# Kernel optimization log

Hardware: AMD Instinct MI355X
Metric: run time of the kernel (lower is better)

## Reference

```python
import jax, jax.numpy as jnp
import numpy as np

N_NODES = 100000
N_EDGES = 1600000
D = 128


def setup_inputs() -> dict:
    key = jax.random.key(0)
    ks = jax.random.split(key, 6)
    x = jax.random.normal(ks[0], (N_NODES, D), dtype=jnp.float32)
    edge_index = jax.random.randint(ks[1], (2, N_EDGES), 0, N_NODES, dtype=jnp.int32)
    # nn.Linear weights: [out, in], bias [out]
    W1 = jax.random.normal(ks[2], (D, D), dtype=jnp.float32) * (1.0 / np.sqrt(D))
    b1 = jax.random.normal(ks[3], (D,), dtype=jnp.float32) * 0.01
    W2 = jax.random.normal(ks[4], (D, D), dtype=jnp.float32) * (1.0 / np.sqrt(D))
    b2 = jax.random.normal(ks[5], (D,), dtype=jnp.float32) * 0.01
    return {"x": x, "edge_index": edge_index, "W1": W1, "b1": b1, "W2": W2, "b2": b2}


def _gin_conv(x, src, dst, W, b, num_nodes):
    # sum aggregation of source features into destination nodes
    agg = jax.ops.segment_sum(x[src], dst, num_segments=num_nodes)  # [N, d]
    # eps = 0 (PyG GINConv default): (1+eps)*x_i + sum_j x_j, then Linear
    return (x + agg) @ W.T + b


def reference(x, edge_index, W1, b1, W2, b2):
    src, dst = edge_index[0], edge_index[1]
    n = x.shape[0]
    hid = _gin_conv(x, src, dst, W1, b1, n)
    out = _gin_conv(hid, src, dst, W2, b2, n)
    return (out, hid)
```

## Files before the change

### kernel.cpp

```cpp
#include <hip/hip_runtime.h>


#define DFEAT 128
#define BSHIFT 8
#define NB_MAX 512
#define CAP 8192
#define LROWS 136

typedef __attribute__((ext_vector_type(8))) short short8;
typedef __attribute__((ext_vector_type(4))) float f32x4;

__device__ __forceinline__ float bf2f(unsigned short u) {
    union { unsigned int i; float f; } c;
    c.i = ((unsigned int)u) << 16;
    return c.f;
}
__device__ __forceinline__ unsigned short f2b(float f) {
    union { float f; unsigned int i; } c;
    c.f = f;
    unsigned int u = c.i;
    u = (u + 0x7FFFu + ((u >> 16) & 1u)) >> 16;
    return (unsigned short)u;
}


__global__ __launch_bounds__(256) void scatter_cast(const int* __restrict__ src,
                                                    const int* __restrict__ dst,
                                                    int* __restrict__ bcur,
                                                    int* __restrict__ ebuf, int E,
                                                    int nscat,
                                                    const float* __restrict__ x,
                                                    unsigned short* __restrict__ xb,
                                                    int total4, int nzero) {
    int tid = threadIdx.x;
    if (blockIdx.x >= nscat) {
        int i = (blockIdx.x - nscat) * 256 + tid;
        if (i < total4) {
            float4 v = ((const float4*)x)[i];
            ushort4 o;
            o.x = f2b(v.x); o.y = f2b(v.y); o.z = f2b(v.z); o.w = f2b(v.w);
            ((ushort4*)xb)[i] = o;
        }
        if (blockIdx.x == nscat && tid < 32)
            ((ushort4*)xb)[(size_t)nzero * 32 + tid] = make_ushort4(0, 0, 0, 0);
        return;
    }
    __shared__ int lh[NB_MAX];
    for (int i = tid; i < NB_MAX; i += 256) lh[i] = 0;
    __syncthreads();
    int e0 = blockIdx.x * 4096;
    int e1 = min(e0 + 4096, E);
    int s[16], d[16];
    #pragma unroll
    for (int j = 0; j < 16; j++) {
        int e = e0 + tid + 256 * j;
        if (e < e1) { s[j] = src[e]; d[j] = dst[e]; atomicAdd(&lh[d[j] >> BSHIFT], 1); }
    }
    __syncthreads();
    for (int i = tid; i < NB_MAX; i += 256) {
        int c = lh[i];
        lh[i] = c ? (i * CAP + atomicAdd(&bcur[i], c)) : 0;
    }
    __syncthreads();
    #pragma unroll
    for (int j = 0; j < 16; j++) {
        int e = e0 + tid + 256 * j;
        if (e < e1) {
            int b = d[j] >> BSHIFT;
            int p = atomicAdd(&lh[b], 1);
            if (p < (b + 1) * CAP) ebuf[p] = (s[j] << 8) | (d[j] & 255);
        }
    }
}


__global__ __launch_bounds__(256) void csr_prep(const int* __restrict__ ebuf,
                                                const int* __restrict__ bcur,
                                                int2* __restrict__ rpse,
                                                int* __restrict__ esrc, int n, int nbk,
                                                const float* __restrict__ W1,
                                                const float* __restrict__ W2,
                                                const float* __restrict__ b1,
                                                unsigned short* __restrict__ Wb1,
                                                unsigned short* __restrict__ Wcb,
                                                float* __restrict__ w2b1) {
    int tid = threadIdx.x;
    if (blockIdx.x >= nbk) {
        __shared__ float red[256];
        int bb = blockIdx.x - nbk;
        int i = bb * 2 + (tid >> 7);
        int j = tid & 127;
        float s = 0.f;
        #pragma unroll 4
        for (int k = 0; k < 128; k++) s += W2[i * 128 + k] * W1[k * 128 + j];
        Wcb[i * 128 + j] = f2b(s);
        Wb1[i * 128 + j] = f2b(W1[i * 128 + j]);
        red[tid] = W2[i * 128 + j] * b1[j];
        __syncthreads();
        if (j == 0) {
            float t = 0.f;
            for (int k = 0; k < 128; k++) t += red[tid + k];
            w2b1[i] = t;
        }
        return;
    }
    __shared__ int hist[256];
    __shared__ int wsum[4];
    __shared__ int woff2[4];
    int b = blockIdx.x;
    int nbase = b << BSHIFT;
    int e0 = b * CAP;
    int e1 = e0 + min(bcur[b], CAP);
    hist[tid] = 0;
    __syncthreads();
    for (int e = e0 + tid; e < e1; e += 256)
        atomicAdd(&hist[ebuf[e] & 255], 1);
    __syncthreads();
    int v = hist[tid];
    int lane = tid & 63, wid = tid >> 6;
    int inc = v;
    #pragma unroll
    for (int off = 1; off < 64; off <<= 1) {
        int u = __shfl_up(inc, off, 64);
        if (lane >= off) inc += u;
    }
    if (lane == 63) wsum[wid] = inc;
    __syncthreads();
    if (tid == 0) {
        int run = 0;
        #pragma unroll
        for (int w = 0; w < 4; w++) { woff2[w] = run; run += wsum[w]; }
    }
    __syncthreads();
    int excl = woff2[wid] + inc - v;
    int node = nbase + tid;
    if (node < n) rpse[node] = make_int2(e0 + excl, e0 + excl + v);
    __syncthreads();
    hist[tid] = excl;
    __syncthreads();
    for (int e = e0 + tid; e < e1; e += 256) {
        int le = ebuf[e];
        int p = atomicAdd(&hist[le & 255], 1);
        esrc[e0 + p] = ((unsigned int)le) >> 8;
    }
}


__device__ __forceinline__ void agg_node16(const char* __restrict__ zb,
                                           const int2* __restrict__ rpse,
                                           const int* __restrict__ esrc,
                                           int node, int nzero, int gl, int gbase,
                                           unsigned lb, float a[8]) {
    int2 se = rpse[node];
    int e0 = se.x, deg = se.y - se.x;
    short8 sv = *(const short8*)(zb + (unsigned)node * 256u + lb);
    #pragma unroll
    for (int t = 0; t < 8; t++) a[t] = bf2f((unsigned short)sv[t]);

    int ei0 = (gl < deg) ? esrc[e0 + gl] : nzero;
    int ei1 = (gl + 16 < deg) ? esrc[e0 + gl + 16] : nzero;

    {
        unsigned off[16];
        short8 vv[16];
        #pragma unroll
        for (int k = 0; k < 16; k++)
            off[k] = (unsigned)__shfl(ei0, gbase + k) * 256u + lb;
        #pragma unroll
        for (int k = 0; k < 16; k++) vv[k] = *(const short8*)(zb + off[k]);
        #pragma unroll
        for (int k = 0; k < 16; k++) {
            #pragma unroll
            for (int t = 0; t < 8; t++) a[t] += bf2f((unsigned short)vv[k][t]);
        }
    }
    if (deg > 16) {
        unsigned off[16];
        short8 vv[16];
        #pragma unroll
        for (int k = 0; k < 16; k++)
            off[k] = (unsigned)__shfl(ei1, gbase + k) * 256u + lb;
        #pragma unroll
        for (int k = 0; k < 16; k++) vv[k] = *(const short8*)(zb + off[k]);
        #pragma unroll
        for (int k = 0; k < 16; k++) {
            #pragma unroll
            for (int t = 0; t < 8; t++) a[t] += bf2f((unsigned short)vv[k][t]);
        }
    }
    for (int rb = 32; rb < deg; rb += 16) {
        int eidx = (rb + gl < deg) ? esrc[e0 + rb + gl] : nzero;
        unsigned off[16];
        short8 vv[16];
        #pragma unroll
        for (int k = 0; k < 16; k++)
            off[k] = (unsigned)__shfl(eidx, gbase + k) * 256u + lb;
        #pragma unroll
        for (int k = 0; k < 16; k++) vv[k] = *(const short8*)(zb + off[k]);
        #pragma unroll
        for (int k = 0; k < 16; k++) {
            #pragma unroll
            for (int t = 0; t < 8; t++) a[t] += bf2f((unsigned short)vv[k][t]);
        }
    }
}

__global__ __launch_bounds__(256) void fused_agg_gemm1(
        const ushort4* __restrict__ zin4, const int2* __restrict__ rpse,
        const int* __restrict__ esrc, const unsigned short* __restrict__ Wb,
        const float* __restrict__ bias, unsigned short* __restrict__ zout,
        float* __restrict__ out, int n) {
    __shared__ __align__(16) short lt[16 * LROWS];
    int nbase = blockIdx.x * 16;
    int w = threadIdx.x >> 6;
    int wl = threadIdx.x & 63;
    int gl = wl & 15, q = wl >> 4;
    int gbase = wl & 48;
    unsigned lb = (unsigned)gl * 16u;
    int lrow = w * 4 + q;
    int node = nbase + lrow;
    const char* zb = (const char*)zin4;

    float a[8];
    #pragma unroll
    for (int t = 0; t < 8; t++) a[t] = 0.f;
    if (node < n) agg_node16(zb, rpse, esrc, node, n, gl, gbase, lb, a);
    short8 o;
    #pragma unroll
    for (int t = 0; t < 8; t++) o[t] = (short)f2b(a[t]);
    *(short8*)((char*)lt + lrow * (LROWS * 2) + lb) = o;
    if (node < n) *(short8*)((char*)zout + (unsigned)node * 256u + lb) = o;
    if (blockIdx.x == 0 && threadIdx.x < 16) {
        short8 z8;
        #pragma unroll
        for (int t = 0; t < 8; t++) z8[t] = 0;
        *(short8*)((char*)zout + (unsigned)n * 256u + threadIdx.x * 16) = z8;
    }
    __syncthreads();

    int m = gl;
    const short* ap = lt + m * LROWS + q * 8;
    short8 a0 = *(const short8*)(ap);
    short8 a1 = *(const short8*)(ap + 32);
    short8 a2 = *(const short8*)(ap + 64);
    short8 a3 = *(const short8*)(ap + 96);
    f32x4 acc[2];
    #pragma unroll
    for (int cc = 0; cc < 2; cc++) acc[cc] = (f32x4){0.f, 0.f, 0.f, 0.f};
    #pragma unroll
    for (int cc = 0; cc < 2; cc++) {
        int c = w * 2 + cc;
        const short* wp = (const short*)Wb + (c * 16 + m) * 128 + q * 8;
        short8 b0 = *(const short8*)(wp);
        short8 b1v = *(const short8*)(wp + 32);
        short8 b2v = *(const short8*)(wp + 64);
        short8 b3v = *(const short8*)(wp + 96);
        acc[cc] = __builtin_amdgcn_mfma_f32_16x16x32_bf16(a0, b0, acc[cc], 0, 0, 0);
        acc[cc] = __builtin_amdgcn_mfma_f32_16x16x32_bf16(a1, b1v, acc[cc], 0, 0, 0);
        acc[cc] = __builtin_amdgcn_mfma_f32_16x16x32_bf16(a2, b2v, acc[cc], 0, 0, 0);
        acc[cc] = __builtin_amdgcn_mfma_f32_16x16x32_bf16(a3, b3v, acc[cc], 0, 0, 0);
    }
    int row0 = nbase + q * 4;
    #pragma unroll
    for (int cc = 0; cc < 2; cc++) {
        int col = (w * 2 + cc) * 16 + m;
        float bb = bias[col];
        #pragma unroll
        for (int r = 0; r < 4; r++) {
            int nd = row0 + r;
            if (nd < n) out[(size_t)nd * 128 + col] = acc[cc][r] + bb;
        }
    }
}

__global__ __launch_bounds__(256) void fused_agg_gemm2(
        const ushort4* __restrict__ zin4, const int2* __restrict__ rpse,
        const int* __restrict__ esrc, const unsigned short* __restrict__ Wb,
        const float* __restrict__ w2b1, const float* __restrict__ bias2,
        float* __restrict__ out, int n) {
    __shared__ __align__(16) short lt[16 * LROWS];
    int nbase = blockIdx.x * 16;
    int w = threadIdx.x >> 6;
    int wl = threadIdx.x & 63;
    int gl = wl & 15, q = wl >> 4;
    int gbase = wl & 48;
    unsigned lb = (unsigned)gl * 16u;
    int lrow = w * 4 + q;
    int node = nbase + lrow;
    const char* zb = (const char*)zin4;

    float a[8];
    #pragma unroll
    for (int t = 0; t < 8; t++) a[t] = 0.f;
    if (node < n) agg_node16(zb, rpse, esrc, node, n, gl, gbase, lb, a);
    short8 o;
    #pragma unroll
    for (int t = 0; t < 8; t++) o[t] = (short)f2b(a[t]);
    *(short8*)((char*)lt + lrow * (LROWS * 2) + lb) = o;
    __syncthreads();

    int m = gl;
    const short* ap = lt + m * LROWS + q * 8;
    short8 a0 = *(const short8*)(ap);
    short8 a1 = *(const short8*)(ap + 32);
    short8 a2 = *(const short8*)(ap + 64);
    short8 a3 = *(const short8*)(ap + 96);
    f32x4 acc[2];
    #pragma unroll
    for (int cc = 0; cc < 2; cc++) acc[cc] = (f32x4){0.f, 0.f, 0.f, 0.f};
    #pragma unroll
    for (int cc = 0; cc < 2; cc++) {
        int c = w * 2 + cc;
        const short* wp = (const short*)Wb + (c * 16 + m) * 128 + q * 8;
        short8 b0 = *(const short8*)(wp);
        short8 b1v = *(const short8*)(wp + 32);
        short8 b2v = *(const short8*)(wp + 64);
        short8 b3v = *(const short8*)(wp + 96);
        acc[cc] = __builtin_amdgcn_mfma_f32_16x16x32_bf16(a0, b0, acc[cc], 0, 0, 0);
        acc[cc] = __builtin_amdgcn_mfma_f32_16x16x32_bf16(a1, b1v, acc[cc], 0, 0, 0);
        acc[cc] = __builtin_amdgcn_mfma_f32_16x16x32_bf16(a2, b2v, acc[cc], 0, 0, 0);
        acc[cc] = __builtin_amdgcn_mfma_f32_16x16x32_bf16(a3, b3v, acc[cc], 0, 0, 0);
    }
    int row0 = nbase + q * 4;
    float degf[4];
    #pragma unroll
    for (int r = 0; r < 4; r++) {
        int nd = row0 + r;
        if (nd < n) {
            int2 se = rpse[nd];
            degf[r] = (float)(1 + se.y - se.x);
        } else degf[r] = 0.f;
    }
    #pragma unroll
    for (int cc = 0; cc < 2; cc++) {
        int col = (w * 2 + cc) * 16 + m;
        float wb = w2b1[col];
        float bb = bias2[col];
        #pragma unroll
        for (int r = 0; r < 4; r++) {
            int nd = row0 + r;
            if (nd < n) out[(size_t)nd * 128 + col] = acc[cc][r] + degf[r] * wb + bb;
        }
    }
}


extern "C" void kernel_launch(void* const* d_in, const int* in_sizes, int n_in,
                              void* d_out, int out_size, void* d_ws, size_t ws_size,
                              hipStream_t stream) {
    const float* x  = (const float*)d_in[0];
    const int*   ei = (const int*)d_in[1];
    const float* W1 = (const float*)d_in[2];
    const float* b1 = (const float*)d_in[3];
    const float* W2 = (const float*)d_in[4];
    const float* b2 = (const float*)d_in[5];

    const int n = in_sizes[0] / DFEAT;
    const int E = in_sizes[1] / 2;
    const int* src = ei;
    const int* dst = ei + E;
    const int nbuckets = (n + (1 << BSHIFT) - 1) >> BSHIFT;

    float* out = (float*)d_out;
    float* hid = out + (size_t)n * DFEAT;

    unsigned short* xb = (unsigned short*)out;

    char* w = (char*)d_ws;
    const size_t szB = (size_t)n * DFEAT * sizeof(unsigned short);
    const size_t szB1 = szB + 4096;
    unsigned short* z1b = (unsigned short*)w;
    int* ebuf = (int*)(w + szB1);
    int* esrc = (int*)(w + szB1 + szB);
    int2* rpse = (int2*)(esrc + (size_t)nbuckets * CAP);
    int* bcur = (int*)(rpse + n);
    char* wp = (char*)(bcur + NB_MAX);
    unsigned short* Wb1 = (unsigned short*)wp;
    unsigned short* Wcb = Wb1 + DFEAT * DFEAT;
    float* w2b1 = (float*)(Wcb + DFEAT * DFEAT);

    const int cast_blocks = (n * 32 + 255) / 256;
    hipMemsetAsync(bcur, 0, nbuckets * sizeof(int), stream);
    scatter_cast<<<nbuckets + cast_blocks, 256, 0, stream>>>(
        src, dst, bcur, ebuf, E, nbuckets, x, xb, n * 32, n);
    csr_prep<<<nbuckets + 64, 256, 0, stream>>>(
        ebuf, bcur, rpse, esrc, n, nbuckets, W1, W2, b1, Wb1, Wcb, w2b1);

    const int fb = (n + 15) / 16;
    fused_agg_gemm1<<<fb, 256, 0, stream>>>(
        (const ushort4*)xb, rpse, esrc, Wb1, b1, z1b, hid, n);
    fused_agg_gemm2<<<fb, 256, 0, stream>>>(
        (const ushort4*)z1b, rpse, esrc, Wcb, w2b1, b2, out, n);
}
```

Measured before the change: 358.4 us.

## Make fused agg-GEMM kernels persistent with prefetch of next tile's CSR indices

Both fused aggregation+GEMM kernels now run as a fixed grid of 2048 blocks that loop over 16-node tiles with a grid stride, instead of one block per tile. Inside the loop, the row-pointer pair and the first 32 neighbour indices for the next tile are loaded while the current tile's gathers are in flight, which hides the dependent index-load latency. Bias values are hoisted out of the loop. The trade-off is extra barriers per tile, more register pressure and fewer blocks available to hide gather latency.

```diff
diff --git a/kernel.cpp b/kernel.cpp
--- a/kernel.cpp
+++ b/kernel.cpp
@@ -6,6 +6,7 @@
 #define NB_MAX 512
 #define CAP 8192
 #define LROWS 136
+#define AGG_BLOCKS 2048
 
 typedef __attribute__((ext_vector_type(8))) short short8;
 typedef __attribute__((ext_vector_type(4))) float f32x4;
@@ -146,130 +147,145 @@
 }
 
 
-__device__ __forceinline__ void agg_node16(const char* __restrict__ zb,
-                                           const int2* __restrict__ rpse,
-                                           const int* __restrict__ esrc,
-                                           int node, int nzero, int gl, int gbase,
-                                           unsigned lb, float a[8]) {
-    int2 se = rpse[node];
-    int e0 = se.x, deg = se.y - se.x;
-    short8 sv = *(const short8*)(zb + (unsigned)node * 256u + lb);
-    #pragma unroll
-    for (int t = 0; t < 8; t++) a[t] = bf2f((unsigned short)sv[t]);
-
-    int ei0 = (gl < deg) ? esrc[e0 + gl] : nzero;
-    int ei1 = (gl + 16 < deg) ? esrc[e0 + gl + 16] : nzero;
-
-    {
-        unsigned off[16];
-        short8 vv[16];
-        #pragma unroll
-        for (int k = 0; k < 16; k++)
-            off[k] = (unsigned)__shfl(ei0, gbase + k) * 256u + lb;
-        #pragma unroll
-        for (int k = 0; k < 16; k++) vv[k] = *(const short8*)(zb + off[k]);
-        #pragma unroll
-        for (int k = 0; k < 16; k++) {
-            #pragma unroll
-            for (int t = 0; t < 8; t++) a[t] += bf2f((unsigned short)vv[k][t]);
-        }
-    }
-    if (deg > 16) {
-        unsigned off[16];
-        short8 vv[16];
-        #pragma unroll
-        for (int k = 0; k < 16; k++)
-            off[k] = (unsigned)__shfl(ei1, gbase + k) * 256u + lb;
-        #pragma unroll
-        for (int k = 0; k < 16; k++) vv[k] = *(const short8*)(zb + off[k]);
-        #pragma unroll
-        for (int k = 0; k < 16; k++) {
-            #pragma unroll
-            for (int t = 0; t < 8; t++) a[t] += bf2f((unsigned short)vv[k][t]);
-        }
-    }
-    for (int rb = 32; rb < deg; rb += 16) {
-        int eidx = (rb + gl < deg) ? esrc[e0 + rb + gl] : nzero;
-        unsigned off[16];
-        short8 vv[16];
-        #pragma unroll
-        for (int k = 0; k < 16; k++)
-            off[k] = (unsigned)__shfl(eidx, gbase + k) * 256u + lb;
-        #pragma unroll
-        for (int k = 0; k < 16; k++) vv[k] = *(const short8*)(zb + off[k]);
-        #pragma unroll
-        for (int k = 0; k < 16; k++) {
-            #pragma unroll
-            for (int t = 0; t < 8; t++) a[t] += bf2f((unsigned short)vv[k][t]);
-        }
-    }
-}
-
 __global__ __launch_bounds__(256) void fused_agg_gemm1(
         const ushort4* __restrict__ zin4, const int2* __restrict__ rpse,
         const int* __restrict__ esrc, const unsigned short* __restrict__ Wb,
         const float* __restrict__ bias, unsigned short* __restrict__ zout,
-        float* __restrict__ out, int n) {
+        float* __restrict__ out, int n, int ntiles) {
     __shared__ __align__(16) short lt[16 * LROWS];
-    int nbase = blockIdx.x * 16;
     int w = threadIdx.x >> 6;
     int wl = threadIdx.x & 63;
     int gl = wl & 15, q = wl >> 4;
     int gbase = wl & 48;
     unsigned lb = (unsigned)gl * 16u;
     int lrow = w * 4 + q;
-    int node = nbase + lrow;
     const char* zb = (const char*)zin4;
-
-    float a[8];
-    #pragma unroll
-    for (int t = 0; t < 8; t++) a[t] = 0.f;
-    if (node < n) agg_node16(zb, rpse, esrc, node, n, gl, gbase, lb, a);
-    short8 o;
-    #pragma unroll
-    for (int t = 0; t < 8; t++) o[t] = (short)f2b(a[t]);
-    *(short8*)((char*)lt + lrow * (LROWS * 2) + lb) = o;
-    if (node < n) *(short8*)((char*)zout + (unsigned)node * 256u + lb) = o;
+    const int stride = gridDim.x;
+
     if (blockIdx.x == 0 && threadIdx.x < 16) {
         short8 z8;
         #pragma unroll
         for (int t = 0; t < 8; t++) z8[t] = 0;
         *(short8*)((char*)zout + (unsigned)n * 256u + threadIdx.x * 16) = z8;
     }
-    __syncthreads();
-
-    int m = gl;
-    const short* ap = lt + m * LROWS + q * 8;
-    short8 a0 = *(const short8*)(ap);
-    short8 a1 = *(const short8*)(ap + 32);
-    short8 a2 = *(const short8*)(ap + 64);
-    short8 a3 = *(const short8*)(ap + 96);
-    f32x4 acc[2];
+
+    float bb[2];
     #pragma unroll
-    for (int cc = 0; cc < 2; cc++) acc[cc] = (f32x4){0.f, 0.f, 0.f, 0.f};
-    #pragma unroll
-    for (int cc = 0; cc < 2; cc++) {
-        int c = w * 2 + cc;
-        const short* wp = (const short*)Wb + (c * 16 + m) * 128 + q * 8;
-        short8 b0 = *(const short8*)(wp);
-        short8 b1v = *(const short8*)(wp + 32);
-        short8 b2v = *(const short8*)(wp + 64);
-        short8 b3v = *(const short8*)(wp + 96);
-        acc[cc] = __builtin_amdgcn_mfma_f32_16x16x32_bf16(a0, b0, acc[cc], 0, 0, 0);
-        acc[cc] = __builtin_amdgcn_mfma_f32_16x16x32_bf16(a1, b1v, acc[cc], 0, 0, 0);
-        acc[cc] = __builtin_amdgcn_mfma_f32_16x16x32_bf16(a2, b2v, acc[cc], 0, 0, 0);
-        acc[cc] = __builtin_amdgcn_mfma_f32_16x16x32_bf16(a3, b3v, acc[cc], 0, 0, 0);
-    }
-    int row0 = nbase + q * 4;
-    #pragma unroll
-    for (int cc = 0; cc < 2; cc++) {
-        int col = (w * 2 + cc) * 16 + m;
-        float bb = bias[col];
-        #pragma unroll
-        for (int r = 0; r < 4; r++) {
-            int nd = row0 + r;
-            if (nd < n) out[(size_t)nd * 128 + col] = acc[cc][r] + bb;
-        }
+    for (int cc = 0; cc < 2; cc++) bb[cc] = bias[(w * 2 + cc) * 16 + gl];
+
+    int t = blockIdx.x;
+    int node = t * 16 + lrow;
+    int2 se = make_int2(0, 0);
+    if (t < ntiles && node < n) se = rpse[node];
+    int deg0 = se.y - se.x;
+    int ei0 = (t < ntiles && node < n && gl < deg0) ? esrc[se.x + gl] : n;
+    int ei1 = (t < ntiles && node < n && gl + 16 < deg0) ? esrc[se.x + gl + 16] : n;
+
+    for (; t < ntiles; ) {
+        int tn = t + stride;
+        int node_n = tn * 16 + lrow;
+        int2 se_n = make_int2(0, 0);
+        if (tn < ntiles && node_n < n) se_n = rpse[node_n];
+
+        int node_c = node < n ? node : n;
+        float a[8];
+        short8 sv = *(const short8*)(zb + (unsigned)node_c * 256u + lb);
+        #pragma unroll
+        for (int tt = 0; tt < 8; tt++) a[tt] = bf2f((unsigned short)sv[tt]);
+
+        unsigned off[16];
+        short8 vv[16];
+        #pragma unroll
+        for (int k = 0; k < 16; k++)
+            off[k] = (unsigned)__shfl(ei0, gbase + k) * 256u + lb;
+        #pragma unroll
+        for (int k = 0; k < 16; k++) vv[k] = *(const short8*)(zb + off[k]);
+
+        int deg_n = se_n.y - se_n.x;
+        int ei0_n = n, ei1_n = n;
+        if (tn < ntiles && node_n < n) {
+            if (gl < deg_n)      ei0_n = esrc[se_n.x + gl];
+            if (gl + 16 < deg_n) ei1_n = esrc[se_n.x + gl + 16];
+        }
+
+        #pragma unroll
+        for (int k = 0; k < 16; k++) {
+            #pragma unroll
+            for (int tt = 0; tt < 8; tt++) a[tt] += bf2f((unsigned short)vv[k][tt]);
+        }
+        int deg = se.y - se.x;
+        if (deg > 16) {
+            unsigned o2[16];
+            short8 v2[16];
+            #pragma unroll
+            for (int k = 0; k < 16; k++)
+                o2[k] = (unsigned)__shfl(ei1, gbase + k) * 256u + lb;
+            #pragma unroll
+            for (int k = 0; k < 16; k++) v2[k] = *(const short8*)(zb + o2[k]);
+            #pragma unroll
+            for (int k = 0; k < 16; k++) {
+                #pragma unroll
+                for (int tt = 0; tt < 8; tt++) a[tt] += bf2f((unsigned short)v2[k][tt]);
+            }
+        }
+        for (int rb = 32; rb < deg; rb += 16) {
+            int eidx = (rb + gl < deg) ? esrc[se.x + rb + gl] : n;
+            unsigned o2[16];
+            short8 v2[16];
+            #pragma unroll
+            for (int k = 0; k < 16; k++)
+                o2[k] = (unsigned)__shfl(eidx, gbase + k) * 256u + lb;
+            #pragma unroll
+            for (int k = 0; k < 16; k++) v2[k] = *(const short8*)(zb + o2[k]);
+            #pragma unroll
+            for (int k = 0; k < 16; k++) {
+                #pragma unroll
+                for (int tt = 0; tt < 8; tt++) a[tt] += bf2f((unsigned short)v2[k][tt]);
+            }
+        }
+
+        short8 o;
+        #pragma unroll
+        for (int tt = 0; tt < 8; tt++) o[tt] = (short)f2b(a[tt]);
+        *(short8*)((char*)lt + lrow * (LROWS * 2) + lb) = o;
+        if (node < n) *(short8*)((char*)zout + (unsigned)node * 256u + lb) = o;
+        __syncthreads();
+
+        int m = gl;
+        const short* ap = lt + m * LROWS + q * 8;
+        short8 a0 = *(const short8*)(ap);
+        short8 a1 = *(const short8*)(ap + 32);
+        short8 a2 = *(const short8*)(ap + 64);
+        short8 a3 = *(const short8*)(ap + 96);
+        f32x4 acc[2];
+        #pragma unroll
+        for (int cc = 0; cc < 2; cc++) acc[cc] = (f32x4){0.f, 0.f, 0.f, 0.f};
+        #pragma unroll
+        for (int cc = 0; cc < 2; cc++) {
+            int c = w * 2 + cc;
+            const short* wp = (const short*)Wb + (c * 16 + m) * 128 + q * 8;
+            short8 b0 = *(const short8*)(wp);
+            short8 b1v = *(const short8*)(wp + 32);
+            short8 b2v = *(const short8*)(wp + 64);
+            short8 b3v = *(const short8*)(wp + 96);
+            acc[cc] = __builtin_amdgcn_mfma_f32_16x16x32_bf16(a0, b0, acc[cc], 0, 0, 0);
+            acc[cc] = __builtin_amdgcn_mfma_f32_16x16x32_bf16(a1, b1v, acc[cc], 0, 0, 0);
+            acc[cc] = __builtin_amdgcn_mfma_f32_16x16x32_bf16(a2, b2v, acc[cc], 0, 0, 0);
+            acc[cc] = __builtin_amdgcn_mfma_f32_16x16x32_bf16(a3, b3v, acc[cc], 0, 0, 0);
+        }
+        int row0 = t * 16 + q * 4;
+        #pragma unroll
+        for (int cc = 0; cc < 2; cc++) {
+            int col = (w * 2 + cc) * 16 + m;
+            #pragma unroll
+            for (int r = 0; r < 4; r++) {
+                int nd = row0 + r;
+                if (nd < n) out[(size_t)nd * 128 + col] = acc[cc][r] + bb[cc];
+            }
+        }
+        __syncthreads();
+
+        se = se_n; ei0 = ei0_n; ei1 = ei1_n; node = node_n; t = tn;
     }
 }
 
@@ -277,70 +293,146 @@
         const ushort4* __restrict__ zin4, const int2* __restrict__ rpse,
         const int* __restrict__ esrc, const unsigned short* __restrict__ Wb,
         const float* __restrict__ w2b1, const float* __restrict__ bias2,
-        float* __restrict__ out, int n) {
+        float* __restrict__ out, int n, int ntiles) {
     __shared__ __align__(16) short lt[16 * LROWS];
-    int nbase = blockIdx.x * 16;
     int w = threadIdx.x >> 6;
     int wl = threadIdx.x & 63;
     int gl = wl & 15, q = wl >> 4;
     int gbase = wl & 48;
     unsigned lb = (unsigned)gl * 16u;
     int lrow = w * 4 + q;
-    int node = nbase + lrow;
     const char* zb = (const char*)zin4;
-
-    float a[8];
-    #pragma unroll
-    for (int t = 0; t < 8; t++) a[t] = 0.f;
-    if (node < n) agg_node16(zb, rpse, esrc, node, n, gl, gbase, lb, a);
-    short8 o;
-    #pragma unroll
-    for (int t = 0; t < 8; t++) o[t] = (short)f2b(a[t]);
-    *(short8*)((char*)lt + lrow * (LROWS * 2) + lb) = o;
-    __syncthreads();
-
-    int m = gl;
-    const short* ap = lt + m * LROWS + q * 8;
-    short8 a0 = *(const short8*)(ap);
-    short8 a1 = *(const short8*)(ap + 32);
-    short8 a2 = *(const short8*)(ap + 64);
-    short8 a3 = *(const short8*)(ap + 96);
-    f32x4 acc[2];
-    #pragma unroll
-    for (int cc = 0; cc < 2; cc++) acc[cc] = (f32x4){0.f, 0.f, 0.f, 0.f};
+    const int stride = gridDim.x;
+
+    float wb2[2], bb2[2];
     #pragma unroll
     for (int cc = 0; cc < 2; cc++) {
-        int c = w * 2 + cc;
-        const short* wp = (const short*)Wb + (c * 16 + m) * 128 + q * 8;
-        short8 b0 = *(const short8*)(wp);
-        short8 b1v = *(const short8*)(wp + 32);
-        short8 b2v = *(const short8*)(wp + 64);
-        short8 b3v = *(const short8*)(wp + 96);
-        acc[cc] = __builtin_amdgcn_mfma_f32_16x16x32_bf16(a0, b0, acc[cc], 0, 0, 0);
-        acc[cc] = __builtin_amdgcn_mfma_f32_16x16x32_bf16(a1, b1v, acc[cc], 0, 0, 0);
-        acc[cc] = __builtin_amdgcn_mfma_f32_16x16x32_bf16(a2, b2v, acc[cc], 0, 0, 0);
-        acc[cc] = __builtin_amdgcn_mfma_f32_16x16x32_bf16(a3, b3v, acc[cc], 0, 0, 0);
-    }
-    int row0 = nbase + q * 4;
-    float degf[4];
-    #pragma unroll
-    for (int r = 0; r < 4; r++) {
-        int nd = row0 + r;
-        if (nd < n) {
-            int2 se = rpse[nd];
-            degf[r] = (float)(1 + se.y - se.x);
-        } else degf[r] = 0.f;
-    }
-    #pragma unroll
-    for (int cc = 0; cc < 2; cc++) {
-        int col = (w * 2 + cc) * 16 + m;
-        float wb = w2b1[col];
-        float bb = bias2[col];
+        int col = (w * 2 + cc) * 16 + gl;
+        wb2[cc] = w2b1[col];
+        bb2[cc] = bias2[col];
+    }
+
+    int t = blockIdx.x;
+    int node = t * 16 + lrow;
+    int2 se = make_int2(0, 0);
+    if (t < ntiles && node < n) se = rpse[node];
+    int deg0 = se.y - se.x;
+    int ei0 = (t < ntiles && node < n && gl < deg0) ? esrc[se.x + gl] : n;
+    int ei1 = (t < ntiles && node < n && gl + 16 < deg0) ? esrc[se.x + gl + 16] : n;
+
+    for (; t < ntiles; ) {
+        int tn = t + stride;
+        int node_n = tn * 16 + lrow;
+        int2 se_n = make_int2(0, 0);
+        if (tn < ntiles && node_n < n) se_n = rpse[node_n];
+
+        int node_c = node < n ? node : n;
+        float a[8];
+        short8 sv = *(const short8*)(zb + (unsigned)node_c * 256u + lb);
+        #pragma unroll
+        for (int tt = 0; tt < 8; tt++) a[tt] = bf2f((unsigned short)sv[tt]);
+
+        unsigned off[16];
+        short8 vv[16];
+        #pragma unroll
+        for (int k = 0; k < 16; k++)
+            off[k] = (unsigned)__shfl(ei0, gbase + k) * 256u + lb;
+        #pragma unroll
+        for (int k = 0; k < 16; k++) vv[k] = *(const short8*)(zb + off[k]);
+
+        int deg_n = se_n.y - se_n.x;
+        int ei0_n = n, ei1_n = n;
+        if (tn < ntiles && node_n < n) {
+            if (gl < deg_n)      ei0_n = esrc[se_n.x + gl];
+            if (gl + 16 < deg_n) ei1_n = esrc[se_n.x + gl + 16];
+        }
+
+        #pragma unroll
+        for (int k = 0; k < 16; k++) {
+            #pragma unroll
+            for (int tt = 0; tt < 8; tt++) a[tt] += bf2f((unsigned short)vv[k][tt]);
+        }
+        int deg = se.y - se.x;
+        if (deg > 16) {
+            unsigned o2[16];
+            short8 v2[16];
+            #pragma unroll
+            for (int k = 0; k < 16; k++)
+                o2[k] = (unsigned)__shfl(ei1, gbase + k) * 256u + lb;
+            #pragma unroll
+            for (int k = 0; k < 16; k++) v2[k] = *(const short8*)(zb + o2[k]);
+            #pragma unroll
+            for (int k = 0; k < 16; k++) {
+                #pragma unroll
+                for (int tt = 0; tt < 8; tt++) a[tt] += bf2f((unsigned short)v2[k][tt]);
+            }
+        }
+        for (int rb = 32; rb < deg; rb += 16) {
+            int eidx = (rb + gl < deg) ? esrc[se.x + rb + gl] : n;
+            unsigned o2[16];
+            short8 v2[16];
+            #pragma unroll
+            for (int k = 0; k < 16; k++)
+                o2[k] = (unsigned)__shfl(eidx, gbase + k) * 256u + lb;
+            #pragma unroll
+            for (int k = 0; k < 16; k++) v2[k] = *(const short8*)(zb + o2[k]);
+            #pragma unroll
+            for (int k = 0; k < 16; k++) {
+                #pragma unroll
+                for (int tt = 0; tt < 8; tt++) a[tt] += bf2f((unsigned short)v2[k][tt]);
+            }
+        }
+
+        short8 o;
+        #pragma unroll
+        for (int tt = 0; tt < 8; tt++) o[tt] = (short)f2b(a[tt]);
+        *(short8*)((char*)lt + lrow * (LROWS * 2) + lb) = o;
+        __syncthreads();
+
+        int m = gl;
+        const short* ap = lt + m * LROWS + q * 8;
+        short8 a0 = *(const short8*)(ap);
+        short8 a1 = *(const short8*)(ap + 32);
+        short8 a2 = *(const short8*)(ap + 64);
+        short8 a3 = *(const short8*)(ap + 96);
+        f32x4 acc[2];
+        #pragma unroll
+        for (int cc = 0; cc < 2; cc++) acc[cc] = (f32x4){0.f, 0.f, 0.f, 0.f};
+        #pragma unroll
+        for (int cc = 0; cc < 2; cc++) {
+            int c = w * 2 + cc;
+            const short* wp = (const short*)Wb + (c * 16 + m) * 128 + q * 8;
+            short8 b0 = *(const short8*)(wp);
+            short8 b1v = *(const short8*)(wp + 32);
+            short8 b2v = *(const short8*)(wp + 64);
+            short8 b3v = *(const short8*)(wp + 96);
+            acc[cc] = __builtin_amdgcn_mfma_f32_16x16x32_bf16(a0, b0, acc[cc], 0, 0, 0);
+            acc[cc] = __builtin_amdgcn_mfma_f32_16x16x32_bf16(a1, b1v, acc[cc], 0, 0, 0);
+            acc[cc] = __builtin_amdgcn_mfma_f32_16x16x32_bf16(a2, b2v, acc[cc], 0, 0, 0);
+            acc[cc] = __builtin_amdgcn_mfma_f32_16x16x32_bf16(a3, b3v, acc[cc], 0, 0, 0);
+        }
+        int row0 = t * 16 + q * 4;
+        float degf[4];
         #pragma unroll
         for (int r = 0; r < 4; r++) {
             int nd = row0 + r;
-            if (nd < n) out[(size_t)nd * 128 + col] = acc[cc][r] + degf[r] * wb + bb;
-        }
+            if (nd < n) {
+                int2 s2 = rpse[nd];
+                degf[r] = (float)(1 + s2.y - s2.x);
+            } else degf[r] = 0.f;
+        }
+        #pragma unroll
+        for (int cc = 0; cc < 2; cc++) {
+            int col = (w * 2 + cc) * 16 + m;
+            #pragma unroll
+            for (int r = 0; r < 4; r++) {
+                int nd = row0 + r;
+                if (nd < n) out[(size_t)nd * 128 + col] = acc[cc][r] + degf[r] * wb2[cc] + bb2[cc];
+            }
+        }
+        __syncthreads();
+
+        se = se_n; ei0 = ei0_n; ei1 = ei1_n; node = node_n; t = tn;
     }
 }
 
@@ -386,9 +478,10 @@
     csr_prep<<<nbuckets + 64, 256, 0, stream>>>(
         ebuf, bcur, rpse, esrc, n, nbuckets, W1, W2, b1, Wb1, Wcb, w2b1);
 
-    const int fb = (n + 15) / 16;
+    const int ntiles = (n + 15) / 16;
+    const int fb = AGG_BLOCKS;
     fused_agg_gemm1<<<fb, 256, 0, stream>>>(
-        (const ushort4*)xb, rpse, esrc, Wb1, b1, z1b, hid, n);
+        (const ushort4*)xb, rpse, esrc, Wb1, b1, z1b, hid, n, ntiles);
     fused_agg_gemm2<<<fb, 256, 0, stream>>>(
-        (const ushort4*)z1b, rpse, esrc, Wcb, w2b1, b2, out, n);
-}
+        (const ushort4*)z1b, rpse, esrc, Wcb, w2b1, b2, out, n, ntiles);
+}
```

Result: faster. 326.2 us (-9.0%).
